# Performance work log

Hardware: AMD Instinct MI355X
Metric: run time of the kernel (lower is better)

Reference implementation:

```python
import jax, jax.numpy as jnp
import numpy as np

SEQ_LEN = 256
NLAYERS = 3
H = 128  # latent_dim == input_dim
OUT_DIM = 2
BATCH = 1024


def setup_inputs() -> dict:
    key = jax.random.key(0)
    ks = jax.random.split(key, 7)
    s = 1.0 / np.sqrt(H)  # PyTorch RNN init scale
    return {
        "hiddens": jax.random.normal(ks[0], (BATCH, NLAYERS, H), jnp.float32),
        "W_ih": jax.random.uniform(ks[1], (NLAYERS, 3 * H, H), jnp.float32, -s, s),
        "W_hh": jax.random.uniform(ks[2], (NLAYERS, 3 * H, H), jnp.float32, -s, s),
        "b_ih": jax.random.uniform(ks[3], (NLAYERS, 3 * H), jnp.float32, -s, s),
        "b_hh": jax.random.uniform(ks[4], (NLAYERS, 3 * H), jnp.float32, -s, s),
        "fc_w": jax.random.uniform(ks[5], (OUT_DIM, H), jnp.float32, -s, s),
        "fc_b": jax.random.uniform(ks[6], (OUT_DIM,), jnp.float32, -s, s),
    }


def _gru_cell(x, h, w_ih, w_hh, bi, bh):
    # x, h: [B, H]; w_*: [3H, H]; b_*: [3H]; PyTorch gate order (r, z, n)
    gx = x @ w_ih.T + bi          # [B, 3H]
    gh = h @ w_hh.T + bh          # [B, 3H]
    xr, xz, xn = jnp.split(gx, 3, axis=-1)
    hr, hz, hn = jnp.split(gh, 3, axis=-1)
    r = jax.nn.sigmoid(xr + hr)
    z = jax.nn.sigmoid(xz + hz)
    n = jnp.tanh(xn + r * hn)
    return (1.0 - z) * n + z * h


def reference(hiddens, W_ih, W_hh, b_ih, b_hh, fc_w, fc_b):
    # hiddens: [B, L, H] -> layer-major [L, B, H] (torch transposes 0,1)
    h = jnp.transpose(hiddens, (1, 0, 2))
    B = hiddens.shape[0]
    x0 = jnp.zeros((B, H), hiddens.dtype)  # torch.zeros initial input

    def step(carry, _):
        x, h = carry
        new_h = []
        inp = x
        for l in range(NLAYERS):
            hl = _gru_cell(inp, h[l], W_ih[l], W_hh[l], b_ih[l], b_hh[l])
            new_h.append(hl)
            inp = hl  # top-layer output feeds next layer / next step
        return (inp, jnp.stack(new_h)), inp

    (_, _), outs = jax.lax.scan(step, (x0, h), None, length=SEQ_LEN)
    outs = jnp.transpose(outs, (1, 0, 2))        # [B, T, H]
    return outs @ fc_w.T + fc_b                  # [B, T, out_dim]
```

## Files before the change

kernel.cpp:

```cpp
#include <hip/hip_runtime.h>
#include <stdint.h>

typedef int   v4i __attribute__((ext_vector_type(4)));
typedef float v4f __attribute__((ext_vector_type(4)));

#define SLOT_SZ  12288
#define LO_OFF   6144
#define BIAS_OFF (2*SLOT_SZ)
#define FC_OFF   (BIAS_OFF + 6144)
#define SMEM_SZ  (FC_OFF + 2048)

#define QW   1436.84056f
#define C1f  4.38394754e-5f
#define C2f  3.45193507e-7f
#define L2E  1.44269504f
#define CR1  (-(L2E)*C1f)
#define CR2  (-(L2E)*C2f)
#define CX1  (2.0f*L2E*C1f)
#define CX2  (2.0f*L2E*C2f)

#define MFMA(A,B,C) __builtin_amdgcn_mfma_i32_16x16x64_i8(A, B, C, 0, 0, 0)

__global__ void prep_weights(const float* __restrict__ Wih,
                             const float* __restrict__ Whh,
                             int8_t* __restrict__ img) {
  int bid = blockIdx.x, lane = threadIdx.x;
  int w = bid / 36, blk = bid % 36;
  int l = blk / 12, rem = blk % 12, o = rem >> 1, kh = rem & 1;
  const float* M = (o & 1) ? Whh : Wih;
  int row = (o >> 1) * 128 + w * 16 + (lane & 15);
  int k0 = kh * 64 + (lane >> 4) * 16;
  const float* src = M + l * 49152 + row * 128 + k0;
  int words[4];
  #pragma unroll
  for (int j4 = 0; j4 < 4; ++j4) {
    unsigned wd = 0;
    #pragma unroll
    for (int j = 0; j < 4; ++j) {
      int q = (int)rintf(src[j4 * 4 + j] * QW);
      wd |= ((unsigned)(q & 255)) << (8 * j);
    }
    words[j4] = (int)wd;
  }
  *(v4i*)(img + (((long)bid) * 64 + lane) * 16) = *(const v4i*)words;
}

#define DECL_ACC v4i aRh={0,0,0,0},aRl={0,0,0,0},aZh={0,0,0,0},aZl={0,0,0,0}, \
                     aXh={0,0,0,0},aXl={0,0,0,0},aHh={0,0,0,0},aHl={0,0,0,0}

#define HMFMA(L,H0,LL0,H1,LL1) do { \
  aRh = MFMA(wr[(L)*12+2],  H0,  aRh);  aRl = MFMA(wr[(L)*12+2],  LL0, aRl); \
  aZh = MFMA(wr[(L)*12+6],  H0,  aZh);  aZl = MFMA(wr[(L)*12+6],  LL0, aZl); \
  aHh = MFMA(wr[(L)*12+10], H0,  aHh);  aHl = MFMA(wr[(L)*12+10], LL0, aHl); \
  aRh = MFMA(wr[(L)*12+3],  H1,  aRh);  aRl = MFMA(wr[(L)*12+3],  LL1, aRl); \
  aZh = MFMA(wr[(L)*12+7],  H1,  aZh);  aZl = MFMA(wr[(L)*12+7],  LL1, aZl); \
  aHh = MFMA(wr[(L)*12+11], H1,  aHh);  aHl = MFMA(wr[(L)*12+11], LL1, aHl); \
} while(0)

#define XMFMA(L,H0,LL0,H1,LL1) do { \
  aRh = MFMA(wr[(L)*12+0],  H0,  aRh);  aRl = MFMA(wr[(L)*12+0],  LL0, aRl); \
  aZh = MFMA(wr[(L)*12+4],  H0,  aZh);  aZl = MFMA(wr[(L)*12+4],  LL0, aZl); \
  aXh = MFMA(wr[(L)*12+8],  H0,  aXh);  aXl = MFMA(wr[(L)*12+8],  LL0, aXl); \
  aRh = MFMA(wr[(L)*12+1],  H1,  aRh);  aRl = MFMA(wr[(L)*12+1],  LL1, aRl); \
  aZh = MFMA(wr[(L)*12+5],  H1,  aZh);  aZl = MFMA(wr[(L)*12+5],  LL1, aZl); \
  aXh = MFMA(wr[(L)*12+9],  H1,  aXh);  aXl = MFMA(wr[(L)*12+9],  LL1, aXl); \
} while(0)

#define EW_WRITE(L, SN, BR, BZ, BX, BH) do { \
  unsigned hiw = 0, low = 0; \
  _Pragma("unroll") \
  for (int r = 0; r < 4; ++r) { \
    float gR = fmaf(CR1, (float)aRh[r], fmaf(CR2, (float)aRl[r], (BR)[r])); \
    float gZ = fmaf(CR1, (float)aZh[r], fmaf(CR2, (float)aZl[r], (BZ)[r])); \
    float gX = fmaf(CX1, (float)aXh[r], fmaf(CX2, (float)aXl[r], (BX)[r])); \
    float gH = fmaf(CX1, (float)aHh[r], fmaf(CX2, (float)aHl[r], (BH)[r])); \
    float rg = __builtin_amdgcn_rcpf(1.f + __builtin_amdgcn_exp2f(gR)); \
    float zg = __builtin_amdgcn_rcpf(1.f + __builtin_amdgcn_exp2f(gZ)); \
    float u  = __builtin_amdgcn_rcpf(1.f + __builtin_amdgcn_exp2f(fmaf(rg, gH, gX))); \
    float ng = fmaf(-2.f, u, 1.f); \
    float hn = fmaf(zg, hst[L][r] - ng, ng); \
    hst[L][r] = hn; \
    float f = hn * 15.875f, fhi = rintf(f); \
    hiw |= ((unsigned)(((int)fhi) & 255)) << (8 * r); \
    low |= ((unsigned)(((int)rintf((f - fhi) * 127.f)) & 255)) << (8 * r); \
  } \
  *(unsigned*)(ewb + (SN) + (L)*2048)          = hiw; \
  *(unsigned*)(ewb + (SN) + (L)*2048 + LO_OFF) = low; \
} while(0)

__global__ __launch_bounds__(512, 1)
void gru_main(const float* __restrict__ hiddens, const float* __restrict__ bih,
              const float* __restrict__ bhh, const float* __restrict__ fcw,
              const float* __restrict__ fcb, const int8_t* __restrict__ img,
              float* __restrict__ out) {
  extern __shared__ char smem[];
  const int tid = threadIdx.x, wg = blockIdx.x;
  const int lane = tid & 63, w = tid >> 6, col = lane & 15, q = lane >> 4;

  v4i wr[36];
  #pragma unroll
  for (int i = 0; i < 36; ++i)
    wr[i] = *(const v4i*)(img + (((long)(w * 36 + i)) * 64 + lane) * 16);

  if (tid < 128) {
    int kh = tid >> 6, ln = tid & 63, c2 = ln & 15, q2 = ln >> 4;
    int words[4] = {0, 0, 0, 0};
    if (c2 < 2) {
      const float* src = fcw + c2 * 128 + kh * 64 + q2 * 16;
      #pragma unroll
      for (int j4 = 0; j4 < 4; ++j4) {
        unsigned wd = 0;
        #pragma unroll
        for (int j = 0; j < 4; ++j) {
          int qv = (int)rintf(src[j4 * 4 + j] * QW);
          wd |= ((unsigned)(qv & 255)) << (8 * j);
        }
        words[j4] = (int)wd;
      }
    }
    *(v4i*)(smem + FC_OFF + kh * 1024 + ln * 16) = *(const v4i*)words;
  }
  for (int i = tid; i < 1536; i += 512) {
    int l = i >> 9, type = (i >> 7) & 3, h = i & 127;
    float bv;
    if      (type == 0) bv = -L2E * (bih[l * 384 + h]       + bhh[l * 384 + h]);
    else if (type == 1) bv = -L2E * (bih[l * 384 + 128 + h] + bhh[l * 384 + 128 + h]);
    else if (type == 2) bv = 2.0f * L2E * bih[l * 384 + 256 + h];
    else                bv = 2.0f * L2E * bhh[l * 384 + 256 + h];
    *(float*)(smem + BIAS_OFF + i * 4) = bv;
  }
  for (int i = tid; i < 6144; i += 512) {
    int l = i >> 11, b = (i >> 7) & 15, h = i & 127;
    float v = hiddens[((long)(wg * 16 + b)) * 384 + l * 128 + h];
    float f = v * 15.875f, fhi = rintf(f);
    int addr = l * 2048 + (h >> 4) * 256 + b * 16 + (h & 15);
    *(int8_t*)(smem + addr)          = (int8_t)(int)fhi;
    *(int8_t*)(smem + addr + LO_OFF) = (int8_t)(int)rintf((f - fhi) * 127.f);
  }
  v4f hst[3];
  #pragma unroll
  for (int l = 0; l < 3; ++l)
    #pragma unroll
    for (int r = 0; r < 4; ++r)
      hst[l][r] = hiddens[((long)(wg * 16 + col)) * 384 + l * 128 + w * 16 + q * 4 + r];

  const float fcb0 = fcb[0], fcb1 = fcb[1];
  __syncthreads();

  const char* fragb = smem + lane * 16;
  char* ewb = smem + w * 256 + col * 16 + q * 4;
  const char* biasb = smem + BIAS_OFF + (w * 16 + q * 4) * 4;

  v4i hh0 = *(const v4i*)(fragb + 0);
  v4i hl0 = *(const v4i*)(fragb + 0 + LO_OFF);
  v4i hh1 = *(const v4i*)(fragb + 1024);
  v4i hl1 = *(const v4i*)(fragb + 1024 + LO_OFF);
  v4i c2h0, c2l0, c2h1, c2l1;

  #pragma unroll 1
  for (int t = 0; t < 256; ++t) {
    const int so = (t & 1) * SLOT_SZ;
    const int sn = SLOT_SZ - so;

    {
      DECL_ACC;
      c2h0 = *(const v4i*)(fragb + so + 2 * 2048);
      c2l0 = *(const v4i*)(fragb + so + 2 * 2048 + LO_OFF);
      c2h1 = *(const v4i*)(fragb + so + 2 * 2048 + 1024);
      c2l1 = *(const v4i*)(fragb + so + 2 * 2048 + 1024 + LO_OFF);
      v4f bRv = *(const v4f*)(biasb + 0 * 512);
      v4f bZv = *(const v4f*)(biasb + 1 * 512);
      v4f bXv = *(const v4f*)(biasb + 2 * 512);
      v4f bHv = *(const v4f*)(biasb + 3 * 512);
      HMFMA(0, hh0, hl0, hh1, hl1);
      if (t > 0) XMFMA(0, c2h0, c2l0, c2h1, c2l1);
      hh0 = *(const v4i*)(fragb + so + 2048);
      hl0 = *(const v4i*)(fragb + so + 2048 + LO_OFF);
      hh1 = *(const v4i*)(fragb + so + 2048 + 1024);
      hl1 = *(const v4i*)(fragb + so + 2048 + 1024 + LO_OFF);
      EW_WRITE(0, sn, bRv, bZv, bXv, bHv);
      __syncthreads();
    }
    {
      DECL_ACC;
      v4i xh0 = *(const v4i*)(fragb + sn + 0);
      v4i xl0 = *(const v4i*)(fragb + sn + 0 + LO_OFF);
      v4i xh1 = *(const v4i*)(fragb + sn + 1024);
      v4i xl1 = *(const v4i*)(fragb + sn + 1024 + LO_OFF);
      v4f bRv = *(const v4f*)(biasb + 4 * 512);
      v4f bZv = *(const v4f*)(biasb + 5 * 512);
      v4f bXv = *(const v4f*)(biasb + 6 * 512);
      v4f bHv = *(const v4f*)(biasb + 7 * 512);
      HMFMA(1, hh0, hl0, hh1, hl1);
      XMFMA(1, xh0, xl0, xh1, xl1);
      EW_WRITE(1, sn, bRv, bZv, bXv, bHv);
      __syncthreads();
    }
    {
      DECL_ACC;
      v4i xh0 = *(const v4i*)(fragb + sn + 2048);
      v4i xl0 = *(const v4i*)(fragb + sn + 2048 + LO_OFF);
      v4i xh1 = *(const v4i*)(fragb + sn + 2048 + 1024);
      v4i xl1 = *(const v4i*)(fragb + sn + 2048 + 1024 + LO_OFF);
      v4f bRv = *(const v4f*)(biasb + 8 * 512);
      v4f bZv = *(const v4f*)(biasb + 9 * 512);
      v4f bXv = *(const v4f*)(biasb + 10 * 512);
      v4f bHv = *(const v4f*)(biasb + 11 * 512);
      HMFMA(2, c2h0, c2l0, c2h1, c2l1);
      XMFMA(2, xh0, xl0, xh1, xl1);
      hh0 = *(const v4i*)(fragb + sn + 0);
      hl0 = *(const v4i*)(fragb + sn + 0 + LO_OFF);
      hh1 = *(const v4i*)(fragb + sn + 1024);
      hl1 = *(const v4i*)(fragb + sn + 1024 + LO_OFF);
      EW_WRITE(2, sn, bRv, bZv, bXv, bHv);
      __syncthreads();
    }
    if (w == 0) {
      v4i dh = {0,0,0,0}, dl = {0,0,0,0};
      #pragma unroll
      for (int kh = 0; kh < 2; ++kh) {
        v4i xh = *(const v4i*)(fragb + sn + 2 * 2048 + kh * 1024);
        v4i xl = *(const v4i*)(fragb + sn + 2 * 2048 + kh * 1024 + LO_OFF);
        v4i fw = *(const v4i*)(smem + FC_OFF + kh * 1024 + lane * 16);
        dh = MFMA(fw, xh, dh);
        dl = MFMA(fw, xl, dl);
      }
      if (q == 0) {
        float2 o2;
        o2.x = fcb0 + C1f * (float)dh[0] + C2f * (float)dl[0];
        o2.y = fcb1 + C1f * (float)dh[1] + C2f * (float)dl[1];
        *(float2*)(out + (((long)(wg * 16 + col)) * 256 + t) * 2) = o2;
      }
    }
  }
}

extern "C" void kernel_launch(void* const* d_in, const int* in_sizes, int n_in,
                              void* d_out, int out_size, void* d_ws, size_t ws_size,
                              hipStream_t stream) {
  (void)in_sizes; (void)n_in; (void)out_size; (void)ws_size;
  const float* hiddens = (const float*)d_in[0];
  const float* Wih     = (const float*)d_in[1];
  const float* Whh     = (const float*)d_in[2];
  const float* bih     = (const float*)d_in[3];
  const float* bhh     = (const float*)d_in[4];
  const float* fcw     = (const float*)d_in[5];
  const float* fcb     = (const float*)d_in[6];
  int8_t* img = (int8_t*)d_ws;
  float* out = (float*)d_out;

  prep_weights<<<288, 64, 0, stream>>>(Wih, Whh, img);
  gru_main<<<64, 512, SMEM_SZ, stream>>>(hiddens, bih, bhh, fcw, fcb, img, out);
}
```

Measured before the change: 775.6 us.

## Defer FC projection into next step's layer-0 phase and pack int8 with v_perm

The FC output projection for step t now runs inside step t+1's first phase, reusing the layer-2 fragments already loaded for the recurrence. It previously ran serially after the last barrier on wave 0, lengthening the critical path. The final step's projection is handled after the loop. Hidden-state fragments are also register-rotated (A/B/C) so layer inputs are not reloaded, and the int8 byte packing uses v_perm instead of shift/or chains. This raises register pressure and adds imbalance to wave 0 during phase 0.

```diff
diff --git a/kernel.cpp b/kernel.cpp
--- a/kernel.cpp
+++ b/kernel.cpp
@@ -67,7 +67,7 @@
 } while(0)
 
 #define EW_WRITE(L, SN, BR, BZ, BX, BH) do { \
-  unsigned hiw = 0, low = 0; \
+  int hi_i[4], lo_i[4]; \
   _Pragma("unroll") \
   for (int r = 0; r < 4; ++r) { \
     float gR = fmaf(CR1, (float)aRh[r], fmaf(CR2, (float)aRl[r], (BR)[r])); \
@@ -81,9 +81,15 @@
     float hn = fmaf(zg, hst[L][r] - ng, ng); \
     hst[L][r] = hn; \
     float f = hn * 15.875f, fhi = rintf(f); \
-    hiw |= ((unsigned)(((int)fhi) & 255)) << (8 * r); \
-    low |= ((unsigned)(((int)rintf((f - fhi) * 127.f)) & 255)) << (8 * r); \
+    hi_i[r] = (int)fhi; \
+    lo_i[r] = (int)rintf((f - fhi) * 127.f); \
   } \
+  unsigned ph01 = __builtin_amdgcn_perm((unsigned)hi_i[1], (unsigned)hi_i[0], 0x00000400u); \
+  unsigned ph23 = __builtin_amdgcn_perm((unsigned)hi_i[3], (unsigned)hi_i[2], 0x04000000u); \
+  unsigned hiw  = __builtin_amdgcn_perm(ph23, ph01, 0x07060100u); \
+  unsigned pl01 = __builtin_amdgcn_perm((unsigned)lo_i[1], (unsigned)lo_i[0], 0x00000400u); \
+  unsigned pl23 = __builtin_amdgcn_perm((unsigned)lo_i[3], (unsigned)lo_i[2], 0x04000000u); \
+  unsigned low  = __builtin_amdgcn_perm(pl23, pl01, 0x07060100u); \
   *(unsigned*)(ewb + (SN) + (L)*2048)          = hiw; \
   *(unsigned*)(ewb + (SN) + (L)*2048 + LO_OFF) = low; \
 } while(0)
@@ -151,11 +157,15 @@
   char* ewb = smem + w * 256 + col * 16 + q * 4;
   const char* biasb = smem + BIAS_OFF + (w * 16 + q * 4) * 4;
 
-  v4i hh0 = *(const v4i*)(fragb + 0);
-  v4i hl0 = *(const v4i*)(fragb + 0 + LO_OFF);
-  v4i hh1 = *(const v4i*)(fragb + 1024);
-  v4i hl1 = *(const v4i*)(fragb + 1024 + LO_OFF);
-  v4i c2h0, c2l0, c2h1, c2l1;
+  v4i Ah0 = *(const v4i*)(fragb + 0);
+  v4i Al0 = *(const v4i*)(fragb + 0 + LO_OFF);
+  v4i Ah1 = *(const v4i*)(fragb + 1024);
+  v4i Al1 = *(const v4i*)(fragb + 1024 + LO_OFF);
+  v4i Bh0 = *(const v4i*)(fragb + 2048);
+  v4i Bl0 = *(const v4i*)(fragb + 2048 + LO_OFF);
+  v4i Bh1 = *(const v4i*)(fragb + 2048 + 1024);
+  v4i Bl1 = *(const v4i*)(fragb + 2048 + 1024 + LO_OFF);
+  v4i Ch0, Cl0, Ch1, Cl1;
 
   #pragma unroll 1
   for (int t = 0; t < 256; ++t) {
@@ -164,73 +174,80 @@
 
     {
       DECL_ACC;
-      c2h0 = *(const v4i*)(fragb + so + 2 * 2048);
-      c2l0 = *(const v4i*)(fragb + so + 2 * 2048 + LO_OFF);
-      c2h1 = *(const v4i*)(fragb + so + 2 * 2048 + 1024);
-      c2l1 = *(const v4i*)(fragb + so + 2 * 2048 + 1024 + LO_OFF);
+      Ch0 = *(const v4i*)(fragb + so + 2 * 2048);
+      Cl0 = *(const v4i*)(fragb + so + 2 * 2048 + LO_OFF);
+      Ch1 = *(const v4i*)(fragb + so + 2 * 2048 + 1024);
+      Cl1 = *(const v4i*)(fragb + so + 2 * 2048 + 1024 + LO_OFF);
       v4f bRv = *(const v4f*)(biasb + 0 * 512);
       v4f bZv = *(const v4f*)(biasb + 1 * 512);
       v4f bXv = *(const v4f*)(biasb + 2 * 512);
       v4f bHv = *(const v4f*)(biasb + 3 * 512);
-      HMFMA(0, hh0, hl0, hh1, hl1);
-      if (t > 0) XMFMA(0, c2h0, c2l0, c2h1, c2l1);
-      hh0 = *(const v4i*)(fragb + so + 2048);
-      hl0 = *(const v4i*)(fragb + so + 2048 + LO_OFF);
-      hh1 = *(const v4i*)(fragb + so + 2048 + 1024);
-      hl1 = *(const v4i*)(fragb + so + 2048 + 1024 + LO_OFF);
+      HMFMA(0, Ah0, Al0, Ah1, Al1);
+      if (t > 0) {
+        XMFMA(0, Ch0, Cl0, Ch1, Cl1);
+        if (w == 0) {
+          v4i dh = {0,0,0,0}, dl = {0,0,0,0};
+          v4i fwA = *(const v4i*)(smem + FC_OFF + 0 * 1024 + lane * 16);
+          v4i fwB = *(const v4i*)(smem + FC_OFF + 1 * 1024 + lane * 16);
+          dh = MFMA(fwA, Ch0, dh);  dl = MFMA(fwA, Cl0, dl);
+          dh = MFMA(fwB, Ch1, dh);  dl = MFMA(fwB, Cl1, dl);
+          if (q == 0) {
+            float2 o2;
+            o2.x = fcb0 + C1f * (float)dh[0] + C2f * (float)dl[0];
+            o2.y = fcb1 + C1f * (float)dh[1] + C2f * (float)dl[1];
+            *(float2*)(out + (((long)(wg * 16 + col)) * 256 + (t - 1)) * 2) = o2;
+          }
+        }
+      }
       EW_WRITE(0, sn, bRv, bZv, bXv, bHv);
       __syncthreads();
     }
     {
       DECL_ACC;
-      v4i xh0 = *(const v4i*)(fragb + sn + 0);
-      v4i xl0 = *(const v4i*)(fragb + sn + 0 + LO_OFF);
-      v4i xh1 = *(const v4i*)(fragb + sn + 1024);
-      v4i xl1 = *(const v4i*)(fragb + sn + 1024 + LO_OFF);
+      Ah0 = *(const v4i*)(fragb + sn + 0);
+      Al0 = *(const v4i*)(fragb + sn + 0 + LO_OFF);
+      Ah1 = *(const v4i*)(fragb + sn + 1024);
+      Al1 = *(const v4i*)(fragb + sn + 1024 + LO_OFF);
       v4f bRv = *(const v4f*)(biasb + 4 * 512);
       v4f bZv = *(const v4f*)(biasb + 5 * 512);
       v4f bXv = *(const v4f*)(biasb + 6 * 512);
       v4f bHv = *(const v4f*)(biasb + 7 * 512);
-      HMFMA(1, hh0, hl0, hh1, hl1);
-      XMFMA(1, xh0, xl0, xh1, xl1);
+      HMFMA(1, Bh0, Bl0, Bh1, Bl1);
+      XMFMA(1, Ah0, Al0, Ah1, Al1);
       EW_WRITE(1, sn, bRv, bZv, bXv, bHv);
       __syncthreads();
     }
     {
       DECL_ACC;
-      v4i xh0 = *(const v4i*)(fragb + sn + 2048);
-      v4i xl0 = *(const v4i*)(fragb + sn + 2048 + LO_OFF);
-      v4i xh1 = *(const v4i*)(fragb + sn + 2048 + 1024);
-      v4i xl1 = *(const v4i*)(fragb + sn + 2048 + 1024 + LO_OFF);
+      Bh0 = *(const v4i*)(fragb + sn + 2048);
+      Bl0 = *(const v4i*)(fragb + sn + 2048 + LO_OFF);
+      Bh1 = *(const v4i*)(fragb + sn + 2048 + 1024);
+      Bl1 = *(const v4i*)(fragb + sn + 2048 + 1024 + LO_OFF);
       v4f bRv = *(const v4f*)(biasb + 8 * 512);
       v4f bZv = *(const v4f*)(biasb + 9 * 512);
       v4f bXv = *(const v4f*)(biasb + 10 * 512);
       v4f bHv = *(const v4f*)(biasb + 11 * 512);
-      HMFMA(2, c2h0, c2l0, c2h1, c2l1);
-      XMFMA(2, xh0, xl0, xh1, xl1);
-      hh0 = *(const v4i*)(fragb + sn + 0);
-      hl0 = *(const v4i*)(fragb + sn + 0 + LO_OFF);
-      hh1 = *(const v4i*)(fragb + sn + 1024);
-      hl1 = *(const v4i*)(fragb + sn + 1024 + LO_OFF);
+      HMFMA(2, Ch0, Cl0, Ch1, Cl1);
+      XMFMA(2, Bh0, Bl0, Bh1, Bl1);
       EW_WRITE(2, sn, bRv, bZv, bXv, bHv);
       __syncthreads();
     }
-    if (w == 0) {
-      v4i dh = {0,0,0,0}, dl = {0,0,0,0};
-      #pragma unroll
-      for (int kh = 0; kh < 2; ++kh) {
-        v4i xh = *(const v4i*)(fragb + sn + 2 * 2048 + kh * 1024);
-        v4i xl = *(const v4i*)(fragb + sn + 2 * 2048 + kh * 1024 + LO_OFF);
-        v4i fw = *(const v4i*)(smem + FC_OFF + kh * 1024 + lane * 16);
-        dh = MFMA(fw, xh, dh);
-        dl = MFMA(fw, xl, dl);
-      }
-      if (q == 0) {
-        float2 o2;
-        o2.x = fcb0 + C1f * (float)dh[0] + C2f * (float)dl[0];
-        o2.y = fcb1 + C1f * (float)dh[1] + C2f * (float)dl[1];
-        *(float2*)(out + (((long)(wg * 16 + col)) * 256 + t) * 2) = o2;
-      }
+  }
+  if (w == 0) {
+    v4i dh = {0,0,0,0}, dl = {0,0,0,0};
+    v4i xh0 = *(const v4i*)(fragb + 2 * 2048);
+    v4i xl0 = *(const v4i*)(fragb + 2 * 2048 + LO_OFF);
+    v4i xh1 = *(const v4i*)(fragb + 2 * 2048 + 1024);
+    v4i xl1 = *(const v4i*)(fragb + 2 * 2048 + 1024 + LO_OFF);
+    v4i fwA = *(const v4i*)(smem + FC_OFF + 0 * 1024 + lane * 16);
+    v4i fwB = *(const v4i*)(smem + FC_OFF + 1 * 1024 + lane * 16);
+    dh = MFMA(fwA, xh0, dh);  dl = MFMA(fwA, xl0, dl);
+    dh = MFMA(fwB, xh1, dh);  dl = MFMA(fwB, xl1, dl);
+    if (q == 0) {
+      float2 o2;
+      o2.x = fcb0 + C1f * (float)dh[0] + C2f * (float)dl[0];
+      o2.y = fcb1 + C1f * (float)dh[1] + C2f * (float)dl[1];
+      *(float2*)(out + (((long)(wg * 16 + col)) * 256 + 255) * 2) = o2;
     }
   }
 }
```

Result: faster. 756.7 us (-2.4%).
